# Kernel optimization log

Measured on AMD Instinct MI355X. Metric: run time of the kernel, lower is better.

The kernel has to match this reference:

```python
import jax, jax.numpy as jnp
import numpy as np

B, S, I, H = 32, 1024, 128, 128
D = 2 * H  # bidirectional concat feature dim


def setup_inputs() -> dict:
    key = jax.random.key(0)
    ks = jax.random.split(key, 12)
    lim = 1.0 / np.sqrt(H)  # PyTorch LSTMCell uniform init bound
    u = lambda k, shape: jax.random.uniform(k, shape, jnp.float32, -lim, lim)
    x = jax.random.normal(ks[0], (B, S, I), jnp.float32)
    return {
        "x": x,
        "fw_Wih": u(ks[1], (4 * H, I)), "fw_Whh": u(ks[2], (4 * H, H)),
        "fw_bih": u(ks[3], (4 * H,)),   "fw_bhh": u(ks[4], (4 * H,)),
        "bw_Wih": u(ks[5], (4 * H, I)), "bw_Whh": u(ks[6], (4 * H, H)),
        "bw_bih": u(ks[7], (4 * H,)),   "bw_bhh": u(ks[8], (4 * H,)),
        "Wq": u(ks[9], (D, D)), "Wk": u(ks[10], (D, D)), "Wv": u(ks[11], (D, D)),
    }


def _lstm_dir(x, Wih, Whh, bih, bhh):
    # x: [B, S, I] -> hidden states [B, S, H]; PyTorch LSTMCell gate math.
    xg = jnp.einsum('bsi,gi->bsg', x, Wih) + bih + bhh  # precompute input projections

    def step(carry, xg_t):
        h, c = carry
        g = xg_t + h @ Whh.T
        i_, f_, g_, o_ = jnp.split(g, 4, axis=-1)
        c = jax.nn.sigmoid(f_) * c + jax.nn.sigmoid(i_) * jnp.tanh(g_)
        h = jax.nn.sigmoid(o_) * jnp.tanh(c)
        return (h, c), h

    h0 = jnp.zeros((x.shape[0], Whh.shape[1]), x.dtype)
    _, hs = jax.lax.scan(step, (h0, h0), jnp.swapaxes(xg, 0, 1))
    return jnp.swapaxes(hs, 0, 1)


def reference(x, fw_Wih, fw_Whh, fw_bih, fw_bhh,
              bw_Wih, bw_Whh, bw_bih, bw_bhh, Wq, Wk, Wv):
    f_h = _lstm_dir(x, fw_Wih, fw_Whh, fw_bih, fw_bhh)            # [B,S,H]
    b_h = _lstm_dir(x[:, ::-1, :], bw_Wih, bw_Whh, bw_bih, bw_bhh)[:, ::-1, :]
    h = jnp.concatenate([f_h, b_h], axis=2)                        # [B,S,2H]
    q = h @ Wq.T
    k = h @ Wk.T
    v = h @ Wv.T
    att = jnp.einsum('bsd,btd->bst', q, k) / jnp.sqrt(jnp.asarray(D, h.dtype))
    att = jax.nn.softmax(att, axis=2)
    return jnp.einsum('bst,btd->bsd', att, v)
```

## Files before the change

kernel.cpp:

```cpp
#include <hip/hip_runtime.h>

typedef unsigned short u16;
typedef unsigned int u32;
typedef __bf16 bf16x8 __attribute__((ext_vector_type(8)));
typedef bf16x8 __attribute__((may_alias)) bf16x8a;
typedef float f32x4 __attribute__((ext_vector_type(4)));
typedef _Float16 f16;
typedef _Float16 f16x2 __attribute__((ext_vector_type(2)));

#define BB 32
#define SS 1024
#define HH 128
#define DD 256

__device__ __forceinline__ float b2f(u16 u) {
    u32 v = ((u32)u) << 16;
    return __builtin_bit_cast(float, v);
}
__device__ __forceinline__ u16 f2b(float f) {
    u32 u = __builtin_bit_cast(u32, f);
    u32 r = (u + 0x7fffu + ((u >> 16) & 1u)) >> 16;
    return (u16)r;
}
__device__ __forceinline__ float sig_fast(float x) {
    return __builtin_amdgcn_rcpf(1.0f + __builtin_amdgcn_exp2f(-1.4426950408889634f * x));
}
__device__ __forceinline__ float tanh_fast(float x) {
    return 2.0f * sig_fast(2.0f * x) - 1.0f;
}

__global__ __launch_bounds__(256) void conv_weights(
    const float* __restrict__ fwWih, const float* __restrict__ bwWih,
    const float* __restrict__ fwWhh, const float* __restrict__ bwWhh,
    const float* __restrict__ Wq, const float* __restrict__ Wk,
    const float* __restrict__ Wv,
    u16* __restrict__ wfih, u16* __restrict__ wbih, u16* __restrict__ whhf,
    u16* __restrict__ wq, u16* __restrict__ wk, u16* __restrict__ wv)
{
    const int which = blockIdx.y;
    const float* src; u16* dst; int mode;
    switch (which) {
        case 0: src = fwWih; dst = wfih;              mode = 0; break;
        case 1: src = bwWih; dst = wbih;              mode = 0; break;
        case 2: src = fwWhh; dst = whhf;              mode = 1; break;
        case 3: src = bwWhh; dst = whhf + 512 * 128;  mode = 1; break;
        case 4: src = Wq;    dst = wq;                mode = 2; break;
        case 5: src = Wk;    dst = wk;                mode = 2; break;
        default: src = Wv;   dst = wv;                mode = 2; break;
    }
    for (int i = blockIdx.x * 256 + threadIdx.x; i < 65536 / 4; i += 32 * 256) {
        float4 v = ((const float4*)src)[i];
        ushort4 o;
        if (mode == 1) {
            o.x = __builtin_bit_cast(u16, (f16)v.x);
            o.y = __builtin_bit_cast(u16, (f16)v.y);
            o.z = __builtin_bit_cast(u16, (f16)v.z);
            o.w = __builtin_bit_cast(u16, (f16)v.w);
        } else {
            o.x = f2b(v.x); o.y = f2b(v.y); o.z = f2b(v.z); o.w = f2b(v.w);
        }
        if (mode == 2) {
            ((ushort4*)dst)[i] = o;
        } else {
            int r = i >> 5, c4 = i & 31;
            int rp = ((r & 127) << 2) | (r >> 7);
            *(ushort4*)&dst[rp * 128 + c4 * 4] = o;
        }
    }
}

template <int MODE, int AFP32>
__device__ __forceinline__ void gemm_core(
    const void* __restrict__ Araw, const u16* __restrict__ Bt,
    const float* __restrict__ bias1, const float* __restrict__ bias2,
    u16* __restrict__ Cout, int K, int N)
{
    __shared__ u16 As[128 * 72];
    __shared__ u16 Bs[128 * 72];
    const int tid = threadIdx.x;
    const int lane = tid & 63, wave = tid >> 6;
    const int wm = wave >> 1, wn = wave & 1;
    const int lo = lane & 15, hi = lane >> 4;
    const int m0 = blockIdx.x * 128, n0 = blockIdx.y * 128;

    f32x4 acc[4][4] = {};

    for (int k0 = 0; k0 < K; k0 += 64) {
        __syncthreads();
#pragma unroll
        for (int i = 0; i < 4; i++) {
            int c = tid + 256 * i;
            int row = c >> 3, kc = (c & 7) * 8;
            if (AFP32) {
                const float* ap = (const float*)Araw + (size_t)(m0 + row) * K + k0 + kc;
                float4 v0 = *(const float4*)ap;
                float4 v1 = *(const float4*)(ap + 4);
                uint4 o;
                o.x = (u32)f2b(v0.x) | ((u32)f2b(v0.y) << 16);
                o.y = (u32)f2b(v0.z) | ((u32)f2b(v0.w) << 16);
                o.z = (u32)f2b(v1.x) | ((u32)f2b(v1.y) << 16);
                o.w = (u32)f2b(v1.z) | ((u32)f2b(v1.w) << 16);
                *(uint4*)&As[row * 72 + kc] = o;
            } else {
                *(uint4*)&As[row * 72 + kc] =
                    *(const uint4*)&((const u16*)Araw)[(size_t)(m0 + row) * K + k0 + kc];
            }
            *(uint4*)&Bs[row * 72 + kc] =
                *(const uint4*)&Bt[(size_t)(n0 + row) * K + k0 + kc];
        }
        __syncthreads();
#pragma unroll
        for (int ks = 0; ks < 2; ks++) {
            bf16x8 af[4], bfr[4];
#pragma unroll
            for (int i = 0; i < 4; i++)
                af[i] = *(const bf16x8a*)&As[(wm * 64 + i * 16 + lo) * 72 + ks * 32 + hi * 8];
#pragma unroll
            for (int j = 0; j < 4; j++)
                bfr[j] = *(const bf16x8a*)&Bs[(wn * 64 + j * 16 + lo) * 72 + ks * 32 + hi * 8];
#pragma unroll
            for (int i = 0; i < 4; i++)
#pragma unroll
                for (int j = 0; j < 4; j++)
                    acc[i][j] = __builtin_amdgcn_mfma_f32_16x16x32_bf16(
                        af[i], bfr[j], acc[i][j], 0, 0, 0);
        }
    }
#pragma unroll
    for (int j = 0; j < 4; j++) {
        int col = n0 + wn * 64 + j * 16 + lo;
        float bsum = 0.f;
        if (MODE == 1) {
            int co = ((col & 3) << 7) | (col >> 2);
            bsum = bias1[co] + bias2[co];
        }
#pragma unroll
        for (int i = 0; i < 4; i++) {
            int row0 = m0 + wm * 64 + i * 16 + hi * 4;
#pragma unroll
            for (int r = 0; r < 4; r++) {
                float v = acc[i][j][r] + bsum;
                if (MODE == 1) {
                    int row = row0 + r;
                    int sidx = row & 1023, bidx = row >> 10;
                    Cout[(size_t)sidx * (BB * 512) + bidx * 512 + col] = f2b(v);
                } else {
                    Cout[(size_t)(row0 + r) * N + col] = f2b(v);
                }
            }
        }
    }
}

__global__ __launch_bounds__(256) void gemm_xg(
    const float* __restrict__ A, const u16* __restrict__ Bt_f,
    const u16* __restrict__ Bt_b,
    const float* __restrict__ f_bih, const float* __restrict__ f_bhh,
    const float* __restrict__ b_bih, const float* __restrict__ b_bhh,
    u16* __restrict__ xg)
{
    const int dir = blockIdx.z;
    gemm_core<1, 1>(A, dir ? Bt_b : Bt_f,
                    dir ? b_bih : f_bih, dir ? b_bhh : f_bhh,
                    xg + (size_t)dir * SS * BB * 512, 128, 512);
}

__global__ __launch_bounds__(256) void gemm_qkv(
    const u16* __restrict__ A, const u16* __restrict__ Wq,
    const u16* __restrict__ Wk, const u16* __restrict__ Wv,
    u16* __restrict__ qb, u16* __restrict__ kb, u16* __restrict__ vb)
{
    const int z = blockIdx.z;
    const u16* Bt = (z == 0) ? Wq : (z == 1) ? Wk : Wv;
    u16* out = (z == 0) ? qb : (z == 1) ? kb : vb;
    gemm_core<0, 0>(A, Bt, nullptr, nullptr, out, 256, 256);
}

__global__ __launch_bounds__(512, 2) void lstm_scan_512(
    const u16* __restrict__ Whh_h,
    const u16* __restrict__ xg,
    u16* __restrict__ hout)
{
    const int wg = blockIdx.x;
    const int dir = wg >> 5, b = wg & 31;
    const int t_ = threadIdx.x;
    const int u = t_ >> 2, g = t_ & 3;

    u32 w[64];
    {
        const uint4* wp = (const uint4*)(Whh_h + (size_t)dir * 512 * 128 + (size_t)t_ * 128);
#pragma unroll
        for (int i = 0; i < 16; i++) {
            uint4 a = wp[i];
            w[4 * i + 0] = a.x; w[4 * i + 1] = a.y;
            w[4 * i + 2] = a.z; w[4 * i + 3] = a.w;
        }
    }

    __shared__ __align__(16) u16 hbuf[2][128];
    if (t_ < 128) hbuf[0][t_] = 0;
    float c = 0.0f;

    const u16* xgp = xg + (size_t)dir * SS * (BB * 512) + (size_t)b * 512 + t_;
    u16* hop = hout + (size_t)b * SS * DD + dir * HH + u;

    int s = dir ? (SS - 1) : 0;
    const int dstep = dir ? -1 : 1;
    u16 xnext = xgp[(size_t)s * (BB * 512)];
    __syncthreads();

    for (int t = 0; t < SS; t++) {
        float xv = b2f(xnext);
        int s_next = s + dstep;
        if (t < SS - 1)
            xnext = xgp[(size_t)s_next * (BB * 512)];

        const uint4* hb = (const uint4*)hbuf[t & 1];
        float p0 = 0.f, p1 = 0.f, p2 = 0.f, p3 = 0.f;
#pragma unroll
        for (int i = 0; i < 16; i++) {
            uint4 hh = hb[i];
            p0 = __builtin_amdgcn_fdot2(__builtin_bit_cast(f16x2, hh.x),
                                        __builtin_bit_cast(f16x2, w[4 * i + 0]), p0, false);
            p1 = __builtin_amdgcn_fdot2(__builtin_bit_cast(f16x2, hh.y),
                                        __builtin_bit_cast(f16x2, w[4 * i + 1]), p1, false);
            p2 = __builtin_amdgcn_fdot2(__builtin_bit_cast(f16x2, hh.z),
                                        __builtin_bit_cast(f16x2, w[4 * i + 2]), p2, false);
            p3 = __builtin_amdgcn_fdot2(__builtin_bit_cast(f16x2, hh.w),
                                        __builtin_bit_cast(f16x2, w[4 * i + 3]), p3, false);
        }
        float sg = ((p0 + p1) + (p2 + p3)) + xv;

        float a1 = __shfl_xor(sg, 1, 64);
        float a2 = __shfl_xor(sg, 2, 64);
        float a3 = __shfl_xor(a1, 2, 64);
        if (g == 0) {
            c = fmaf(sig_fast(a1), c, sig_fast(sg) * tanh_fast(a2));
            float h = sig_fast(a3) * tanh_fast(c);
            hbuf[(t + 1) & 1][u] = __builtin_bit_cast(u16, (f16)h);
            hop[(size_t)s * DD] = f2b(h);
        }
        __syncthreads();
        s = s_next;
    }
}

__global__ __launch_bounds__(256) void transpose_v(
    const u16* __restrict__ v, u16* __restrict__ vT)
{
    __shared__ u16 tile[64 * 72];
    const int b = blockIdx.z, s0 = blockIdx.x * 64, d0 = blockIdx.y * 64;
    const int tid = threadIdx.x;
#pragma unroll
    for (int i = 0; i < 2; i++) {
        int c = tid + 256 * i;
        int sl = c >> 3, dc = (c & 7) * 8;
        *(uint4*)&tile[sl * 72 + dc] =
            *(const uint4*)&v[((size_t)b * SS + s0 + sl) * DD + d0 + dc];
    }
    __syncthreads();
#pragma unroll
    for (int i = 0; i < 2; i++) {
        int c = tid + 256 * i;
        int dl = c >> 3, sc = (c & 7) * 8;
        u32 x0 = (u32)tile[(sc + 0) * 72 + dl] | ((u32)tile[(sc + 1) * 72 + dl] << 16);
        u32 x1 = (u32)tile[(sc + 2) * 72 + dl] | ((u32)tile[(sc + 3) * 72 + dl] << 16);
        u32 x2 = (u32)tile[(sc + 4) * 72 + dl] | ((u32)tile[(sc + 5) * 72 + dl] << 16);
        u32 x3 = (u32)tile[(sc + 6) * 72 + dl] | ((u32)tile[(sc + 7) * 72 + dl] << 16);
        uint4 val; val.x = x0; val.y = x1; val.z = x2; val.w = x3;
        *(uint4*)&vT[((size_t)b * DD + d0 + dl) * SS + s0 + sc] = val;
    }
}

__global__ __launch_bounds__(256) void attn_kernel(
    const u16* __restrict__ q, const u16* __restrict__ k,
    const u16* __restrict__ vT, float* __restrict__ out)
{
    __shared__ u16 Ks[32 * 264];
    __shared__ u16 Vs[256 * 40];
    __shared__ u16 Ps[64 * 40];
    const int b = blockIdx.y, q0 = blockIdx.x * 64;
    const int tid = threadIdx.x, wave = tid >> 6, lane = tid & 63;
    const int lo = lane & 15, hi = lane >> 4;
    const float c1 = 0.09016844005556021f;

    bf16x8 qf[8];
    {
        const u16* qp = q + ((size_t)b * SS + q0 + wave * 16 + lo) * DD;
#pragma unroll
        for (int ks = 0; ks < 8; ks++)
            qf[ks] = *(const bf16x8a*)&qp[ks * 32 + hi * 8];
    }
    float m_i[4] = {-1e30f, -1e30f, -1e30f, -1e30f};
    float l_i[4] = {0.f, 0.f, 0.f, 0.f};
    f32x4 o[16] = {};

    for (int t0 = 0; t0 < SS; t0 += 32) {
        __syncthreads();
#pragma unroll
        for (int i = 0; i < 4; i++) {
            int c = tid + 256 * i;
            {
                int row = c >> 5, dc = (c & 31) * 8;
                *(uint4*)&Ks[row * 264 + dc] =
                    *(const uint4*)&k[((size_t)b * SS + t0 + row) * DD + dc];
            }
            {
                int d = c >> 2, sc = (c & 3) * 8;
                *(uint4*)&Vs[d * 40 + sc] =
                    *(const uint4*)&vT[((size_t)b * DD + d) * SS + t0 + sc];
            }
        }
        __syncthreads();

        f32x4 sacc[2] = {};
#pragma unroll
        for (int ks = 0; ks < 8; ks++) {
#pragma unroll
            for (int j = 0; j < 2; j++) {
                bf16x8 bfr = *(const bf16x8a*)&Ks[(j * 16 + lo) * 264 + ks * 32 + hi * 8];
                sacc[j] = __builtin_amdgcn_mfma_f32_16x16x32_bf16(qf[ks], bfr, sacc[j], 0, 0, 0);
            }
        }

        float tt[2][4];
#pragma unroll
        for (int j = 0; j < 2; j++)
#pragma unroll
            for (int r = 0; r < 4; r++) tt[j][r] = sacc[j][r] * c1;
        float rm[4];
#pragma unroll
        for (int r = 0; r < 4; r++) rm[r] = fmaxf(tt[0][r], tt[1][r]);
#pragma unroll
        for (int mm = 1; mm <= 8; mm <<= 1)
#pragma unroll
            for (int r = 0; r < 4; r++) rm[r] = fmaxf(rm[r], __shfl_xor(rm[r], mm, 64));
        float al[4], rs[4];
#pragma unroll
        for (int r = 0; r < 4; r++) {
            float mn = fmaxf(m_i[r], rm[r]);
            al[r] = __builtin_amdgcn_exp2f(m_i[r] - mn);
            m_i[r] = mn;
            rs[r] = 0.f;
        }
#pragma unroll
        for (int j = 0; j < 2; j++)
#pragma unroll
            for (int r = 0; r < 4; r++) {
                float p = __builtin_amdgcn_exp2f(tt[j][r] - m_i[r]);
                rs[r] += p;
                Ps[(wave * 16 + hi * 4 + r) * 40 + j * 16 + lo] = f2b(p);
            }
#pragma unroll
        for (int mm = 1; mm <= 8; mm <<= 1)
#pragma unroll
            for (int r = 0; r < 4; r++) rs[r] += __shfl_xor(rs[r], mm, 64);
#pragma unroll
        for (int r = 0; r < 4; r++) l_i[r] = l_i[r] * al[r] + rs[r];
#pragma unroll
        for (int nt = 0; nt < 16; nt++) {
            o[nt][0] *= al[0]; o[nt][1] *= al[1];
            o[nt][2] *= al[2]; o[nt][3] *= al[3];
        }
        __syncthreads();
        bf16x8 pa = *(const bf16x8a*)&Ps[(wave * 16 + lo) * 40 + hi * 8];
#pragma unroll
        for (int nt = 0; nt < 16; nt++) {
            bf16x8 bv = *(const bf16x8a*)&Vs[(nt * 16 + lo) * 40 + hi * 8];
            o[nt] = __builtin_amdgcn_mfma_f32_16x16x32_bf16(pa, bv, o[nt], 0, 0, 0);
        }
    }
    float inv[4];
#pragma unroll
    for (int r = 0; r < 4; r++) inv[r] = __builtin_amdgcn_rcpf(l_i[r]);
#pragma unroll
    for (int nt = 0; nt < 16; nt++)
#pragma unroll
        for (int r = 0; r < 4; r++) {
            int row = q0 + wave * 16 + hi * 4 + r;
            int col = nt * 16 + lo;
            out[((size_t)b * SS + row) * DD + col] = o[nt][r] * inv[r];
        }
}

extern "C" void kernel_launch(void* const* d_in, const int* in_sizes, int n_in,
                              void* d_out, int out_size, void* d_ws, size_t ws_size,
                              hipStream_t stream)
{
    (void)in_sizes; (void)n_in; (void)out_size;
    const float* x      = (const float*)d_in[0];
    const float* fw_Wih = (const float*)d_in[1];
    const float* fw_Whh = (const float*)d_in[2];
    const float* fw_bih = (const float*)d_in[3];
    const float* fw_bhh = (const float*)d_in[4];
    const float* bw_Wih = (const float*)d_in[5];
    const float* bw_Whh = (const float*)d_in[6];
    const float* bw_bih = (const float*)d_in[7];
    const float* bw_bhh = (const float*)d_in[8];
    const float* Wq = (const float*)d_in[9];
    const float* Wk = (const float*)d_in[10];
    const float* Wv = (const float*)d_in[11];

    if (ws_size < 143523840ULL) return;

    char* ws = (char*)d_ws;
    u16* xg  = (u16*)ws;
    u16* h   = (u16*)(ws + 67108864);
    u16* qb  = (u16*)(ws + 83886080);
    u16* kb  = (u16*)(ws + 100663296);
    u16* vT  = (u16*)(ws + 117440512);
    u16* wfih16 = (u16*)(ws + 142606336);
    u16* wbih16 = (u16*)(ws + 142606336 + 131072);
    u16* wq16   = (u16*)(ws + 142606336 + 262144);
    u16* wk16   = (u16*)(ws + 142606336 + 393216);
    u16* wv16   = (u16*)(ws + 142606336 + 524288);
    u16* whhf16 = (u16*)(ws + 142606336 + 655360);
    u16* vb = (u16*)ws;

    conv_weights<<<dim3(32, 7), 256, 0, stream>>>(
        fw_Wih, bw_Wih, fw_Whh, bw_Whh, Wq, Wk, Wv,
        wfih16, wbih16, whhf16, wq16, wk16, wv16);

    gemm_xg<<<dim3(256, 4, 2), 256, 0, stream>>>(
        x, wfih16, wbih16, fw_bih, fw_bhh, bw_bih, bw_bhh, xg);
    lstm_scan_512<<<64, 512, 0, stream>>>(whhf16, xg, h);
    gemm_qkv<<<dim3(256, 2, 3), 256, 0, stream>>>(h, wq16, wk16, wv16, qb, kb, vb);
    transpose_v<<<dim3(16, 4, 32), 256, 0, stream>>>(vb, vT);
    attn_kernel<<<dim3(16, 32), 256, 0, stream>>>(qb, kb, vT, (float*)d_out);
}
```

Measured before the change: 899.3 us.

## Split LSTM scan work by hidden unit and K-half across 256 threads

The recurrent LSTM scan kernel now uses 256 threads per block instead of 512. Each thread owns all four gates of one hidden unit for half of the K dimension, and the two halves are combined with one shuffle. This removes the three cross-lane gate shuffles and the g==0 divergence, so every lane does the gate math and the two lanes of a pair split the h writes. In exchange each thread keeps 128 weight registers instead of 64, and the weights are loaded through volatile scalar reads, which adds register pressure and setup cost.

After: 837.1 us. 6.9% less time.

```diff
diff --git a/kernel.cpp b/kernel.cpp
--- a/kernel.cpp
+++ b/kernel.cpp
@@ -176,7 +176,7 @@
     gemm_core<0, 0>(A, Bt, nullptr, nullptr, out, 256, 256);
 }
 
-__global__ __launch_bounds__(512, 2) void lstm_scan_512(
+__global__ __launch_bounds__(256, 1) void lstm_scan_sk(
     const u16* __restrict__ Whh_h,
     const u16* __restrict__ xg,
     u16* __restrict__ hout)
@@ -184,16 +184,17 @@
     const int wg = blockIdx.x;
     const int dir = wg >> 5, b = wg & 31;
     const int t_ = threadIdx.x;
-    const int u = t_ >> 2, g = t_ & 3;
-
-    u32 w[64];
+    const int u = t_ >> 1;
+    const int kh = t_ & 1;
+
+    u32 w[4][32];
     {
-        const uint4* wp = (const uint4*)(Whh_h + (size_t)dir * 512 * 128 + (size_t)t_ * 128);
-#pragma unroll
-        for (int i = 0; i < 16; i++) {
-            uint4 a = wp[i];
-            w[4 * i + 0] = a.x; w[4 * i + 1] = a.y;
-            w[4 * i + 2] = a.z; w[4 * i + 3] = a.w;
+        const volatile u32* vp = (const volatile u32*)(Whh_h + (size_t)dir * 512 * 128);
+#pragma unroll
+        for (int g = 0; g < 4; g++) {
+            int base = ((4 * u + g) * 128 + kh * 64) >> 1;
+#pragma unroll
+            for (int k = 0; k < 32; k++) w[g][k] = vp[base + k];
         }
     }
 
@@ -201,45 +202,49 @@
     if (t_ < 128) hbuf[0][t_] = 0;
     float c = 0.0f;
 
-    const u16* xgp = xg + (size_t)dir * SS * (BB * 512) + (size_t)b * 512 + t_;
+    const u16* xgp = xg + (size_t)dir * SS * (BB * 512) + (size_t)b * 512 + 4 * u;
     u16* hop = hout + (size_t)b * SS * DD + dir * HH + u;
 
     int s = dir ? (SS - 1) : 0;
     const int dstep = dir ? -1 : 1;
-    u16 xnext = xgp[(size_t)s * (BB * 512)];
+    uint2 nx = *(const uint2*)&xgp[(size_t)s * (BB * 512)];
     __syncthreads();
 
     for (int t = 0; t < SS; t++) {
-        float xv = b2f(xnext);
+        uint2 xv = nx;
         int s_next = s + dstep;
         if (t < SS - 1)
-            xnext = xgp[(size_t)s_next * (BB * 512)];
-
-        const uint4* hb = (const uint4*)hbuf[t & 1];
-        float p0 = 0.f, p1 = 0.f, p2 = 0.f, p3 = 0.f;
-#pragma unroll
-        for (int i = 0; i < 16; i++) {
-            uint4 hh = hb[i];
-            p0 = __builtin_amdgcn_fdot2(__builtin_bit_cast(f16x2, hh.x),
-                                        __builtin_bit_cast(f16x2, w[4 * i + 0]), p0, false);
-            p1 = __builtin_amdgcn_fdot2(__builtin_bit_cast(f16x2, hh.y),
-                                        __builtin_bit_cast(f16x2, w[4 * i + 1]), p1, false);
-            p2 = __builtin_amdgcn_fdot2(__builtin_bit_cast(f16x2, hh.z),
-                                        __builtin_bit_cast(f16x2, w[4 * i + 2]), p2, false);
-            p3 = __builtin_amdgcn_fdot2(__builtin_bit_cast(f16x2, hh.w),
-                                        __builtin_bit_cast(f16x2, w[4 * i + 3]), p3, false);
-        }
-        float sg = ((p0 + p1) + (p2 + p3)) + xv;
-
-        float a1 = __shfl_xor(sg, 1, 64);
-        float a2 = __shfl_xor(sg, 2, 64);
-        float a3 = __shfl_xor(a1, 2, 64);
-        if (g == 0) {
-            c = fmaf(sig_fast(a1), c, sig_fast(sg) * tanh_fast(a2));
-            float h = sig_fast(a3) * tanh_fast(c);
+            nx = *(const uint2*)&xgp[(size_t)s_next * (BB * 512)];
+
+        const uint4* hb = (const uint4*)&hbuf[t & 1][kh * 64];
+        float g0 = 0.f, g1 = 0.f, g2 = 0.f, g3 = 0.f;
+#pragma unroll
+        for (int cc = 0; cc < 8; cc++) {
+            uint4 hh = hb[cc];
+            u32 hv[4] = {hh.x, hh.y, hh.z, hh.w};
+#pragma unroll
+            for (int j = 0; j < 4; j++) {
+                f16x2 hp = __builtin_bit_cast(f16x2, hv[j]);
+                g0 = __builtin_amdgcn_fdot2(hp, __builtin_bit_cast(f16x2, w[0][4 * cc + j]), g0, false);
+                g1 = __builtin_amdgcn_fdot2(hp, __builtin_bit_cast(f16x2, w[1][4 * cc + j]), g1, false);
+                g2 = __builtin_amdgcn_fdot2(hp, __builtin_bit_cast(f16x2, w[2][4 * cc + j]), g2, false);
+                g3 = __builtin_amdgcn_fdot2(hp, __builtin_bit_cast(f16x2, w[3][4 * cc + j]), g3, false);
+            }
+        }
+        g0 += __shfl_xor(g0, 1, 64);
+        g1 += __shfl_xor(g1, 1, 64);
+        g2 += __shfl_xor(g2, 1, 64);
+        g3 += __shfl_xor(g3, 1, 64);
+        g0 += b2f((u16)(xv.x & 0xffff)); g1 += b2f((u16)(xv.x >> 16));
+        g2 += b2f((u16)(xv.y & 0xffff)); g3 += b2f((u16)(xv.y >> 16));
+
+        c = fmaf(sig_fast(g1), c, sig_fast(g0) * tanh_fast(g2));
+        float h = sig_fast(g3) * tanh_fast(c);
+
+        if (kh == 0)
             hbuf[(t + 1) & 1][u] = __builtin_bit_cast(u16, (f16)h);
+        else
             hop[(size_t)s * DD] = f2b(h);
-        }
         __syncthreads();
         s = s_next;
     }
@@ -423,7 +428,7 @@
 
     gemm_xg<<<dim3(256, 4, 2), 256, 0, stream>>>(
         x, wfih16, wbih16, fw_bih, fw_bhh, bw_bih, bw_bhh, xg);
-    lstm_scan_512<<<64, 512, 0, stream>>>(whhf16, xg, h);
+    lstm_scan_sk<<<64, 256, 0, stream>>>(whhf16, xg, h);
     gemm_qkv<<<dim3(256, 2, 3), 256, 0, stream>>>(h, wq16, wk16, wv16, qb, kb, vb);
     transpose_v<<<dim3(16, 4, 32), 256, 0, stream>>>(vb, vT);
     attn_kernel<<<dim3(16, 32), 256, 0, stream>>>(qb, kb, vT, (float*)d_out);
```
